# Optimization experiments

Hardware: AMD Instinct MI355X
Metric: run time of the kernel (lower is better)

The kernel has to match this reference:

```python
import jax, jax.numpy as jnp
import numpy as np

B, D, NUM_HOP, NUM_REL = 8192, 512, 8, 2000  # batch, input_dim, num_hop, num_relation
TAU = 1.0


def setup_inputs() -> dict:
    key = jax.random.key(0)
    ks = jax.random.split(key, 7)
    s = 1.0 / np.sqrt(D)  # PyTorch GRU uniform init bound
    return {
        "query": jax.random.normal(ks[0], (B, D), jnp.float32),
        "W_ih": jax.random.uniform(ks[1], (3 * D, D), jnp.float32, -s, s),
        "W_hh": jax.random.uniform(ks[2], (3 * D, D), jnp.float32, -s, s),
        "b_ih": jax.random.uniform(ks[3], (3 * D,), jnp.float32, -s, s),
        "b_hh": jax.random.uniform(ks[4], (3 * D,), jnp.float32, -s, s),
        "relation": jax.random.normal(ks[5], (2 * NUM_REL, D), jnp.float32),
        "eos": jax.random.normal(ks[6], (1, D), jnp.float32),
    }


def gru_cell(x, h, W_ih, W_hh, b_ih, b_hh):
    # PyTorch nn.GRU cell, gate order (r, z, n)
    gi = x @ W_ih.T + b_ih  # [B, 3D]
    gh = h @ W_hh.T + b_hh  # [B, 3D]
    ir, iz, i_n = jnp.split(gi, 3, axis=-1)
    hr, hz, h_n = jnp.split(gh, 3, axis=-1)
    r = jax.nn.sigmoid(ir + hr)
    z = jax.nn.sigmoid(iz + hz)
    n = jnp.tanh(i_n + r * h_n)
    return (1.0 - z) * n + z * h


def reference(query, W_ih, W_hh, b_ih, b_hh, relation, eos):
    # gru over seq [query, eos] starting from h0 = 0; hidden[1:] == final hx for 1 layer
    h0 = jnp.zeros_like(query)
    h1 = gru_cell(query, h0, W_ih, W_hh, b_ih, b_hh)
    hidden = gru_cell(jnp.broadcast_to(eos, query.shape), h1, W_ih, W_hh, b_ih, b_hh)

    def step(h, _):
        score = jnp.einsum('bd,rd->br', h, relation)          # [B, 2R]
        attention = jax.nn.softmax(score / TAU, axis=-1)
        subgoal = jnp.einsum('br,rd->bd', attention, relation)  # [B, D]
        h_new = gru_cell(subgoal, h, W_ih, W_hh, b_ih, b_hh)
        return h_new, subgoal

    _, subgoals = jax.lax.scan(step, hidden, None, length=NUM_HOP)  # [NUM_HOP, B, D]
    subgoals = jnp.moveaxis(subgoals, 0, 1)  # [B, NUM_HOP, D]
    masks = jnp.ones(subgoals.shape[:-1], dtype=bool)
    return subgoals, masks
```

## Files before the change

### kernel.cpp

```cpp
#include <hip/hip_runtime.h>


typedef _Float16 f16;
typedef _Float16 f16x8 __attribute__((ext_vector_type(8)));
typedef _Float16 f16x4 __attribute__((ext_vector_type(4)));
typedef float    f32x4 __attribute__((ext_vector_type(4)));

constexpr int BATCH = 8192;
constexpr int DDIM  = 512;
constexpr int D3    = 1536;
constexpr int NRELT = 4000;
constexpr int NRELP = 4096;
constexpr int NHOP  = 8;

#define MFMA16(a,b,c) __builtin_amdgcn_mfma_f32_16x16x32_f16((a),(b),(c),0,0,0)
#define BAR()   __builtin_amdgcn_s_barrier()
#define FENCE() asm volatile("" ::: "memory")
#define SCHED0() __builtin_amdgcn_sched_barrier(0)
#define VM(n) asm volatile("s_waitcnt vmcnt(" #n ")" ::: "memory")

__device__ __forceinline__ void gll16(const void* g, void* l) {
  __builtin_amdgcn_global_load_lds(
      (const __attribute__((address_space(1))) unsigned int*)g,
      (__attribute__((address_space(3))) unsigned int*)l, 16, 0, 0);
}

__global__ __launch_bounds__(256) void k_split(const float* __restrict__ src,
                                               f16* __restrict__ hi, f16* __restrict__ lo, int n) {
  int i = blockIdx.x * 256 + threadIdx.x;
  if (i >= n) return;
  float v = src[i];
  f16 h = (f16)v;
  hi[i] = h;
  lo[i] = (f16)(v - (float)h);
}

__global__ __launch_bounds__(256) void k_prep_rel(const float* __restrict__ rel,
    f16* __restrict__ rhi, f16* __restrict__ rlo,
    f16* __restrict__ thi, f16* __restrict__ tlo) {
  int i = blockIdx.x * 256 + threadIdx.x;
  if (i >= NRELP * DDIM) return;
  int r = i >> 9, d = i & 511;
  float v = (r < NRELT) ? rel[i] : 0.f;
  f16 h = (f16)v, l = (f16)(v - (float)h);
  rhi[i] = h; rlo[i] = l;
  thi[(size_t)d * NRELP + r] = h;
  tlo[(size_t)d * NRELP + r] = l;
}

__global__ __launch_bounds__(64) void k_gieos(const float* __restrict__ W,
                                              const float* __restrict__ eos,
                                              float* __restrict__ out) {
  int o = blockIdx.x;
  float s = 0.f;
  for (int i = threadIdx.x; i < DDIM; i += 64) s += W[(size_t)o * DDIM + i] * eos[i];
  for (int off = 32; off; off >>= 1) s += __shfl_xor(s, off);
  if (threadIdx.x == 0) out[o] = s;
}

#define MQUAD(AOP, BOP, FMOFF) \
  __builtin_amdgcn_s_setprio(1); \
  _Pragma("unroll") \
  for (int fm = 0; fm < 4; ++fm) { \
    _Pragma("unroll") \
    for (int fn = 0; fn < 4; ++fn) \
      acc[(FMOFF) + fm][fn] = MFMA16(AOP[fm], BOP[fn], acc[(FMOFF) + fm][fn]); \
  } \
  __builtin_amdgcn_s_setprio(0); \
  SCHED0();

template<int EPI>
__device__ __forceinline__ void gemm_core(
    const f16* __restrict__ Ahi, const f16* __restrict__ Alo, int lda,
    const f16* __restrict__ Bhi, const f16* __restrict__ Blo, int ldb,
    float* __restrict__ Cout, f16* __restrict__ Chi, f16* __restrict__ Clo,
    int ldc, int m0, int n0, int kst, int nt, f16* lds)
{
  const int tid  = threadIdx.x;
  const int lane = tid & 63;
  const int wave = tid >> 6;
  const int wm = wave >> 2;
  const int wn = wave & 3;
  const int rb = lane & 15;
  const int sl = lane >> 4;
  const int srow = lane >> 2;

  auto stage2 = [&](int buf, int p, int k0) {
    const f16* src = (p == 0) ? Ahi : (p == 1) ? Alo : (p == 2) ? Bhi : Blo;
    const int ld   = (p < 2) ? lda : ldb;
    const int base = (p < 2) ? m0 : n0;
    f16* pl = lds + ((buf * 4 + p) << 13);
    #pragma unroll
    for (int c = 0; c < 2; ++c) {
      const int r0 = wave * 16 + c * 128;
      const int lr = r0 + srow;
      const int slot = (lane & 3) ^ ((lr >> 1) & 3);
      gll16(src + (size_t)(base + lr) * ld + k0 + slot * 8, pl + r0 * 32);
    }
  };
  auto rd = [&](int buf, int p, int lr) -> f16x8 {
    const int off = lr * 64 + ((sl ^ ((lr >> 1) & 3)) << 4);
    return *(const f16x8*)((const char*)(lds + ((buf * 4 + p) << 13)) + off);
  };

  stage2(0, 2, kst); stage2(0, 0, kst); stage2(0, 1, kst); stage2(0, 3, kst);

  f32x4 acc[8][4] = {};
  f16x8 ah[4], al[4], bh[4], bl[4];
  const int A0 = wm * 128, B0 = wn * 64;

  for (int t = 0; t < nt; ++t) {
    const int cur = t & 1;
    const int nxt = cur ^ 1;
    const bool more = (t + 1 < nt);
    const int kn = kst + (t + 1) * 32;

    if (more) { stage2(nxt, 2, kn); VM(6); } else { VM(4); }
    FENCE(); BAR(); FENCE();
    #pragma unroll
    for (int f = 0; f < 4; ++f) ah[f] = rd(cur, 0, A0 + f * 16 + rb);
    #pragma unroll
    for (int f = 0; f < 4; ++f) bh[f] = rd(cur, 2, B0 + f * 16 + rb);
    FENCE(); BAR(); FENCE();
    MQUAD(ah, bh, 0)

    if (more) { stage2(nxt, 0, kn); VM(6); } else { VM(2); }
    FENCE(); BAR(); FENCE();
    #pragma unroll
    for (int f = 0; f < 4; ++f) al[f] = rd(cur, 1, A0 + f * 16 + rb);
    FENCE(); BAR(); FENCE();
    MQUAD(al, bh, 0)

    if (more) { stage2(nxt, 1, kn); VM(6); } else { VM(0); }
    FENCE(); BAR(); FENCE();
    #pragma unroll
    for (int f = 0; f < 4; ++f) bl[f] = rd(cur, 3, B0 + f * 16 + rb);
    FENCE(); BAR(); FENCE();
    MQUAD(ah, bl, 0)

    if (more) stage2(nxt, 3, kn);
    FENCE(); BAR(); FENCE();
    #pragma unroll
    for (int f = 0; f < 4; ++f) ah[f] = rd(cur, 0, A0 + 64 + f * 16 + rb);
    FENCE(); BAR(); FENCE();
    MQUAD(ah, bl, 4)

    FENCE(); BAR(); FENCE();
    MQUAD(ah, bh, 4)

    FENCE(); BAR(); FENCE();
    #pragma unroll
    for (int f = 0; f < 4; ++f) al[f] = rd(cur, 1, A0 + 64 + f * 16 + rb);
    FENCE(); BAR(); FENCE();
    MQUAD(al, bh, 4)
  }

  #pragma unroll
  for (int fm = 0; fm < 8; ++fm)
    #pragma unroll
    for (int fn = 0; fn < 4; ++fn)
      #pragma unroll
      for (int r = 0; r < 4; ++r) {
        const int gr = m0 + wm * 128 + fm * 16 + sl * 4 + r;
        const int gc = n0 + wn * 64 + fn * 16 + rb;
        const float v = acc[fm][fn][r];
        if constexpr (EPI == 0) {
          Cout[(size_t)gr * ldc + gc] = v;
        } else {
          const f16 vh = (f16)v;
          Chi[(size_t)gr * ldc + gc] = vh;
          Clo[(size_t)gr * ldc + gc] = (f16)(v - (float)vh);
        }
      }
}

template<int EPI>
__global__ __launch_bounds__(512, 2)
void k_gemm8(const f16* __restrict__ Ahi, const f16* __restrict__ Alo, int lda,
             const f16* __restrict__ Bhi, const f16* __restrict__ Blo, int ldb,
             float* __restrict__ Cout, f16* __restrict__ Chi, f16* __restrict__ Clo,
             int ldc, int K, int gy, int nblocks)
{
  __shared__ __align__(16) f16 lds[2 * 4 * 256 * 32];
  const int bid = blockIdx.x;
  const int id2 = (bid & 7) * (nblocks >> 3) + (bid >> 3);
  const int m = id2 & 31;
  const int rest = id2 >> 5;
  const int n = rest % gy;
  const int z = rest / gy;
  float* Co = Cout ? Cout + (size_t)z * BATCH * (size_t)ldc : nullptr;
  gemm_core<EPI>(Ahi, Alo, lda, Bhi, Blo, ldb, Co, Chi, Clo, ldc,
                 m * 256, n * 256, z * K, K / 32, lds);
}

__global__ __launch_bounds__(512, 2)
void k_gemm8_gru(const f16* __restrict__ xhi, const f16* __restrict__ xlo,
                 const f16* __restrict__ hhi, const f16* __restrict__ hlo,
                 const f16* __restrict__ wihhi, const f16* __restrict__ wihlo,
                 const f16* __restrict__ whhhi, const f16* __restrict__ whhlo,
                 float* __restrict__ gi, float* __restrict__ gh)
{
  __shared__ __align__(16) f16 lds[2 * 4 * 256 * 32];
  const int bid = blockIdx.x;
  const int id2 = (bid & 7) * 48 + (bid >> 3);
  const int m = id2 & 31;
  const int nn = id2 >> 5;
  const bool second = nn >= 6;
  gemm_core<0>(second ? hhi : xhi, second ? hlo : xlo, DDIM,
               second ? whhhi : wihhi, second ? whhlo : wihlo, DDIM,
               second ? gh : gi, nullptr, nullptr, D3,
               m * 256, (second ? nn - 6 : nn) * 256, 0, DDIM / 32, lds);
}

__global__ __launch_bounds__(256)
void k_softmax(f16* __restrict__ Shi, f16* __restrict__ Slo) {
  const int row = blockIdx.x;
  f16* phi = Shi + (size_t)row * NRELP;
  f16* plo = Slo + (size_t)row * NRELP;
  const int tid = threadIdx.x, lane = tid & 63, wv = tid >> 6;
  const int ng = (tid < 232) ? 4 : 3;
  f32x4 v[4];
  float mx = -3.402823e38f;
  #pragma unroll
  for (int i = 0; i < 4; ++i)
    if (i < ng) {
      f16x4 hv = *(const f16x4*)(phi + (tid + 256 * i) * 4);
      f16x4 lv = *(const f16x4*)(plo + (tid + 256 * i) * 4);
      #pragma unroll
      for (int j = 0; j < 4; ++j) v[i][j] = (float)hv[j] + (float)lv[j];
      mx = fmaxf(fmaxf(fmaxf(mx, v[i][0]), fmaxf(v[i][1], v[i][2])), v[i][3]);
    }
  float l = 0.f;
  #pragma unroll
  for (int i = 0; i < 4; ++i)
    if (i < ng)
      l += __expf(v[i][0] - mx) + __expf(v[i][1] - mx)
         + __expf(v[i][2] - mx) + __expf(v[i][3] - mx);
  #pragma unroll
  for (int off = 1; off < 64; off <<= 1) {
    float om = __shfl_xor(mx, off), ol = __shfl_xor(l, off);
    float nm = fmaxf(mx, om);
    l = l * __expf(mx - nm) + ol * __expf(om - nm);
    mx = nm;
  }
  __shared__ float sm[4], slr[4];
  if (lane == 0) { sm[wv] = mx; slr[wv] = l; }
  __syncthreads();
  const float fm = fmaxf(fmaxf(sm[0], sm[1]), fmaxf(sm[2], sm[3]));
  const float fl = slr[0] * __expf(sm[0] - fm) + slr[1] * __expf(sm[1] - fm)
                 + slr[2] * __expf(sm[2] - fm) + slr[3] * __expf(sm[3] - fm);
  const float il = 1.f / fl;
  #pragma unroll
  for (int i = 0; i < 4; ++i)
    if (i < ng) {
      f16x4 oh, ol;
      #pragma unroll
      for (int j = 0; j < 4; ++j) {
        const float pv = __expf(v[i][j] - fm) * il;
        const f16 ph = (f16)pv;
        oh[j] = ph;
        ol[j] = (f16)(pv - (float)ph);
      }
      *(f16x4*)(phi + (tid + 256 * i) * 4) = oh;
      *(f16x4*)(plo + (tid + 256 * i) * 4) = ol;
    }
  if (tid < 24) {
    f16x4 z = {(f16)0.f, (f16)0.f, (f16)0.f, (f16)0.f};
    *(f16x4*)(phi + (1000 + tid) * 4) = z;
    *(f16x4*)(plo + (1000 + tid) * 4) = z;
  }
}

__global__ __launch_bounds__(256)
void k_subred(const float* __restrict__ Cp, float* __restrict__ outp,
              f16* __restrict__ xhi, f16* __restrict__ xlo, int hop) {
  const int idx = blockIdx.x * 256 + threadIdx.x;
  const int b = idx >> 7, d4 = (idx & 127) * 4;
  const size_t o = (size_t)b * DDIM + d4;
  f32x4 s = *(const f32x4*)(Cp + o);
  s += *(const f32x4*)(Cp + (size_t)BATCH * DDIM + o);
  s += *(const f32x4*)(Cp + 2 * (size_t)BATCH * DDIM + o);
  s += *(const f32x4*)(Cp + 3 * (size_t)BATCH * DDIM + o);
  *(f32x4*)(outp + (size_t)b * (NHOP * DDIM) + (size_t)hop * DDIM + d4) = s;
  f16x4 vh, vl;
  #pragma unroll
  for (int j = 0; j < 4; ++j) {
    const f16 ph = (f16)s[j];
    vh[j] = ph;
    vl[j] = (f16)(s[j] - (float)ph);
  }
  *(f16x4*)(xhi + o) = vh;
  *(f16x4*)(xlo + o) = vl;
}

__global__ __launch_bounds__(256)
void k_gates(const float* __restrict__ gi, const float* __restrict__ givec,
             const float* __restrict__ gh,
             const float* __restrict__ bih, const float* __restrict__ bhh,
             const float* __restrict__ hin, float* __restrict__ hout,
             f16* __restrict__ hhi, f16* __restrict__ hlo)
{
  const int idx = blockIdx.x * 256 + threadIdx.x;
  const int b  = idx >> 7;
  const int d4 = (idx & 127) * 4;
  f32x4 ir, iz, inn;
  if (gi) {
    const float* g = gi + (size_t)b * D3 + d4;
    ir  = *(const f32x4*)(g);
    iz  = *(const f32x4*)(g + DDIM);
    inn = *(const f32x4*)(g + 2 * DDIM);
  } else {
    ir  = *(const f32x4*)(givec + d4);
    iz  = *(const f32x4*)(givec + DDIM + d4);
    inn = *(const f32x4*)(givec + 2 * DDIM + d4);
  }
  ir  += *(const f32x4*)(bih + d4);
  iz  += *(const f32x4*)(bih + DDIM + d4);
  inn += *(const f32x4*)(bih + 2 * DDIM + d4);
  f32x4 hr = {0.f, 0.f, 0.f, 0.f}, hz = {0.f, 0.f, 0.f, 0.f}, hn = {0.f, 0.f, 0.f, 0.f};
  if (gh) {
    const float* g = gh + (size_t)b * D3 + d4;
    hr = *(const f32x4*)(g);
    hz = *(const f32x4*)(g + DDIM);
    hn = *(const f32x4*)(g + 2 * DDIM);
  }
  hr += *(const f32x4*)(bhh + d4);
  hz += *(const f32x4*)(bhh + DDIM + d4);
  hn += *(const f32x4*)(bhh + 2 * DDIM + d4);
  f32x4 hp = {0.f, 0.f, 0.f, 0.f};
  if (hin) hp = *(const f32x4*)(hin + (size_t)b * DDIM + d4);
  f32x4 hv; f16x4 vh, vl;
  #pragma unroll
  for (int j = 0; j < 4; ++j) {
    const float r = 1.f / (1.f + __expf(-(ir[j] + hr[j])));
    const float z = 1.f / (1.f + __expf(-(iz[j] + hz[j])));
    const float n = tanhf(inn[j] + r * hn[j]);
    const float h = (1.f - z) * n + z * hp[j];
    hv[j] = h;
    const f16 ph = (f16)h;
    vh[j] = ph;
    vl[j] = (f16)(h - (float)ph);
  }
  *(f32x4*)(hout + (size_t)b * DDIM + d4) = hv;
  *(f16x4*)(hhi + (size_t)b * DDIM + d4) = vh;
  *(f16x4*)(hlo + (size_t)b * DDIM + d4) = vl;
}

__global__ __launch_bounds__(256) void k_ones(float* __restrict__ o, int n) {
  int i = blockIdx.x * 256 + threadIdx.x;
  if (i < n) o[i] = 1.0f;
}

extern "C" void kernel_launch(void* const* d_in, const int* in_sizes, int n_in,
                              void* d_out, int out_size, void* d_ws, size_t ws_size,
                              hipStream_t stream)
{
  const float* query = (const float*)d_in[0];
  const float* W_ih  = (const float*)d_in[1];
  const float* W_hh  = (const float*)d_in[2];
  const float* b_ih  = (const float*)d_in[3];
  const float* b_hh  = (const float*)d_in[4];
  const float* rel   = (const float*)d_in[5];
  const float* eos   = (const float*)d_in[6];
  float* out = (float*)d_out;
  (void)in_sizes; (void)n_in; (void)out_size; (void)ws_size;

  char* w = (char*)d_ws;
  f16* SPhi    = (f16*)w;   w += (size_t)BATCH * NRELP * 2;
  f16* SPlo    = (f16*)w;   w += (size_t)BATCH * NRELP * 2;
  float* Cpart = (float*)w; w += (size_t)4 * BATCH * DDIM * 4;
  float* hbuf  = (float*)w; w += (size_t)BATCH * DDIM * 4;
  f16* h_hi    = (f16*)w;   w += (size_t)BATCH * DDIM * 2;
  f16* h_lo    = (f16*)w;   w += (size_t)BATCH * DDIM * 2;
  f16* x_hi    = (f16*)w;   w += (size_t)BATCH * DDIM * 2;
  f16* x_lo    = (f16*)w;   w += (size_t)BATCH * DDIM * 2;
  f16* wih_hi  = (f16*)w;   w += (size_t)D3 * DDIM * 2;
  f16* wih_lo  = (f16*)w;   w += (size_t)D3 * DDIM * 2;
  f16* whh_hi  = (f16*)w;   w += (size_t)D3 * DDIM * 2;
  f16* whh_lo  = (f16*)w;   w += (size_t)D3 * DDIM * 2;
  f16* rel_hi  = (f16*)w;   w += (size_t)NRELP * DDIM * 2;
  f16* rel_lo  = (f16*)w;   w += (size_t)NRELP * DDIM * 2;
  f16* relT_hi = (f16*)w;   w += (size_t)DDIM * NRELP * 2;
  f16* relT_lo = (f16*)w;   w += (size_t)DDIM * NRELP * 2;
  float* gieos = (float*)w; w += (size_t)D3 * 4;
  float* gi = (float*)SPhi;
  float* gh = (float*)SPhi + (size_t)BATCH * D3;

  k_split<<<(BATCH * DDIM + 255) / 256, 256, 0, stream>>>(query, x_hi, x_lo, BATCH * DDIM);
  k_split<<<(D3 * DDIM + 255) / 256, 256, 0, stream>>>(W_ih, wih_hi, wih_lo, D3 * DDIM);
  k_split<<<(D3 * DDIM + 255) / 256, 256, 0, stream>>>(W_hh, whh_hi, whh_lo, D3 * DDIM);
  k_prep_rel<<<(NRELP * DDIM + 255) / 256, 256, 0, stream>>>(rel, rel_hi, rel_lo, relT_hi, relT_lo);
  k_gieos<<<D3, 64, 0, stream>>>(W_ih, eos, gieos);

  const int ggrid = BATCH * DDIM / 4 / 256;

  k_gemm8<0><<<192, 512, 0, stream>>>(x_hi, x_lo, DDIM, wih_hi, wih_lo, DDIM,
      gi, nullptr, nullptr, D3, DDIM, 6, 192);
  k_gates<<<ggrid, 256, 0, stream>>>(gi, nullptr, nullptr, b_ih, b_hh, nullptr, hbuf, h_hi, h_lo);

  k_gemm8<0><<<192, 512, 0, stream>>>(h_hi, h_lo, DDIM, whh_hi, whh_lo, DDIM,
      gh, nullptr, nullptr, D3, DDIM, 6, 192);
  k_gates<<<ggrid, 256, 0, stream>>>(nullptr, gieos, gh, b_ih, b_hh, hbuf, hbuf, h_hi, h_lo);

  for (int hop = 0; hop < NHOP; ++hop) {
    k_gemm8<1><<<512, 512, 0, stream>>>(h_hi, h_lo, DDIM, rel_hi, rel_lo, DDIM,
        nullptr, SPhi, SPlo, NRELP, DDIM, 16, 512);
    k_softmax<<<BATCH, 256, 0, stream>>>(SPhi, SPlo);
    k_gemm8<0><<<256, 512, 0, stream>>>(SPhi, SPlo, NRELP,
        relT_hi, relT_lo, NRELP, Cpart, nullptr, nullptr, DDIM, 1024, 2, 256);
    k_subred<<<ggrid, 256, 0, stream>>>(Cpart, out, x_hi, x_lo, hop);
    k_gemm8_gru<<<384, 512, 0, stream>>>(x_hi, x_lo, h_hi, h_lo,
        wih_hi, wih_lo, whh_hi, whh_lo, gi, gh);
    k_gates<<<ggrid, 256, 0, stream>>>(gi, nullptr, gh, b_ih, b_hh, hbuf, hbuf, h_hi, h_lo);
  }

  k_ones<<<(BATCH * NHOP + 255) / 256, 256, 0, stream>>>(out + (size_t)BATCH * NHOP * DDIM, BATCH * NHOP);
}
```

Measured before the change: 3.129 ms.

## Restructure split-fp16 GEMM main loop into three phases with fewer barriers

Reorganizes the hi/lo split-precision GEMM inner loop from six quarter-tile MFMA phases with many barriers into three full-tile phases (ah*bh, al*bh, ah*bl). Each phase loads all 8 A fragments at once and covers the whole 8x4 accumulator tile. Next-stage prefetches are regrouped, with A-hi and B-hi issued together, and the wait counts are adjusted to match. The aim is to cut barrier and synchronization overhead and give longer uninterrupted MFMA streams, at the cost of more VGPRs for the fragment arrays, which could reduce occupancy or cause spills.

```diff
diff --git a/kernel.cpp b/kernel.cpp
--- a/kernel.cpp
+++ b/kernel.cpp
@@ -57,17 +57,6 @@
   for (int off = 32; off; off >>= 1) s += __shfl_xor(s, off);
   if (threadIdx.x == 0) out[o] = s;
 }
-
-#define MQUAD(AOP, BOP, FMOFF) \
-  __builtin_amdgcn_s_setprio(1); \
-  _Pragma("unroll") \
-  for (int fm = 0; fm < 4; ++fm) { \
-    _Pragma("unroll") \
-    for (int fn = 0; fn < 4; ++fn) \
-      acc[(FMOFF) + fm][fn] = MFMA16(AOP[fm], BOP[fn], acc[(FMOFF) + fm][fn]); \
-  } \
-  __builtin_amdgcn_s_setprio(0); \
-  SCHED0();
 
 template<int EPI>
 __device__ __forceinline__ void gemm_core(
@@ -103,10 +92,10 @@
     return *(const f16x8*)((const char*)(lds + ((buf * 4 + p) << 13)) + off);
   };
 
-  stage2(0, 2, kst); stage2(0, 0, kst); stage2(0, 1, kst); stage2(0, 3, kst);
+  stage2(0, 0, kst); stage2(0, 2, kst); stage2(0, 1, kst); stage2(0, 3, kst);
 
   f32x4 acc[8][4] = {};
-  f16x8 ah[4], al[4], bh[4], bl[4];
+  f16x8 ah[8], al[8], bh[4], bl[4];
   const int A0 = wm * 128, B0 = wn * 64;
 
   for (int t = 0; t < nt; ++t) {
@@ -115,44 +104,46 @@
     const bool more = (t + 1 < nt);
     const int kn = kst + (t + 1) * 32;
 
-    if (more) { stage2(nxt, 2, kn); VM(6); } else { VM(4); }
-    FENCE(); BAR(); FENCE();
-    #pragma unroll
-    for (int f = 0; f < 4; ++f) ah[f] = rd(cur, 0, A0 + f * 16 + rb);
+    if (more) { stage2(nxt, 0, kn); stage2(nxt, 2, kn); VM(8); } else { VM(4); }
+    BAR(); FENCE();
+    #pragma unroll
+    for (int f = 0; f < 8; ++f) ah[f] = rd(cur, 0, A0 + f * 16 + rb);
     #pragma unroll
     for (int f = 0; f < 4; ++f) bh[f] = rd(cur, 2, B0 + f * 16 + rb);
-    FENCE(); BAR(); FENCE();
-    MQUAD(ah, bh, 0)
-
-    if (more) { stage2(nxt, 0, kn); VM(6); } else { VM(2); }
-    FENCE(); BAR(); FENCE();
-    #pragma unroll
-    for (int f = 0; f < 4; ++f) al[f] = rd(cur, 1, A0 + f * 16 + rb);
-    FENCE(); BAR(); FENCE();
-    MQUAD(al, bh, 0)
-
-    if (more) { stage2(nxt, 1, kn); VM(6); } else { VM(0); }
-    FENCE(); BAR(); FENCE();
+    __builtin_amdgcn_s_setprio(1);
+    #pragma unroll
+    for (int m = 0; m < 8; ++m)
+      #pragma unroll
+      for (int n = 0; n < 4; ++n)
+        acc[m][n] = MFMA16(ah[m], bh[n], acc[m][n]);
+    __builtin_amdgcn_s_setprio(0);
+    SCHED0();
+
+    if (more) { stage2(nxt, 1, kn); VM(8); } else { VM(2); }
+    BAR(); FENCE();
+    #pragma unroll
+    for (int f = 0; f < 8; ++f) al[f] = rd(cur, 1, A0 + f * 16 + rb);
+    __builtin_amdgcn_s_setprio(1);
+    #pragma unroll
+    for (int m = 0; m < 8; ++m)
+      #pragma unroll
+      for (int n = 0; n < 4; ++n)
+        acc[m][n] = MFMA16(al[m], bh[n], acc[m][n]);
+    __builtin_amdgcn_s_setprio(0);
+    SCHED0();
+
+    if (more) { stage2(nxt, 3, kn); VM(8); } else { VM(0); }
+    BAR(); FENCE();
     #pragma unroll
     for (int f = 0; f < 4; ++f) bl[f] = rd(cur, 3, B0 + f * 16 + rb);
-    FENCE(); BAR(); FENCE();
-    MQUAD(ah, bl, 0)
-
-    if (more) stage2(nxt, 3, kn);
-    FENCE(); BAR(); FENCE();
-    #pragma unroll
-    for (int f = 0; f < 4; ++f) ah[f] = rd(cur, 0, A0 + 64 + f * 16 + rb);
-    FENCE(); BAR(); FENCE();
-    MQUAD(ah, bl, 4)
-
-    FENCE(); BAR(); FENCE();
-    MQUAD(ah, bh, 4)
-
-    FENCE(); BAR(); FENCE();
-    #pragma unroll
-    for (int f = 0; f < 4; ++f) al[f] = rd(cur, 1, A0 + 64 + f * 16 + rb);
-    FENCE(); BAR(); FENCE();
-    MQUAD(al, bh, 4)
+    __builtin_amdgcn_s_setprio(1);
+    #pragma unroll
+    for (int m = 0; m < 8; ++m)
+      #pragma unroll
+      for (int n = 0; n < 4; ++n)
+        acc[m][n] = MFMA16(ah[m], bl[n], acc[m][n]);
+    __builtin_amdgcn_s_setprio(0);
+    SCHED0();
   }
 
   #pragma unroll
```

Result: faster. 3.041 ms (-2.8%).
